# Performance work log

Hardware: AMD Instinct MI355X
Metric: run time of the kernel (lower is better)

The kernel has to match this reference:

```python
import jax, jax.numpy as jnp
import numpy as np

N, E, B = 10000, 160000, 16
IN, H, A, L, OUT = 16, 64, 8, 2, 1
MSG_IN = 2 * (H + 1) + 1   # 131 = concat(x_i, x_j, additional_message_features)
UPD_IN = H + 1 + H         # 129 = concat(x_aug, aggregated message)


def _tp(h, a, W, b):
    # scalar-irreps fully-connected O3 tensor product == bilinear map + bias
    return jnp.einsum('ni,nj,ijk->nk', h, a, W) + b


def setup_inputs() -> dict:
    key = jax.random.key(0)
    ks = jax.random.split(key, 24)
    f32 = jnp.float32
    def rn(k, shape, scale=1.0):
        return jax.random.normal(k, shape, f32) * scale
    def w(k, shape):
        fan = shape[-3] * shape[-2]
        return rn(k, shape, 1.0 / np.sqrt(fan))
    return {
        'x': rn(ks[0], (N, IN)),
        'edge_index': jax.random.randint(ks[1], (2, E), 0, N),
        'edge_attr': rn(ks[2], (E, A)),
        'node_attr': rn(ks[3], (N, A)),
        'additional_message_features': rn(ks[4], (E, 1)),
        'additional_node_features': rn(ks[5], (N, 1)),
        'batch': jnp.sort(jax.random.randint(ks[6], (N,), 0, B)),
        'W_emb': w(ks[7], (IN + 1, A, H)), 'b_emb': jnp.zeros((H,), f32),
        'Wm1': w(ks[8], (L, MSG_IN, A, H)), 'bm1': jnp.zeros((L, H), f32),
        'Wm2': w(ks[9], (L, H, A, H)), 'bm2': jnp.zeros((L, H), f32),
        'Wu1': w(ks[10], (L, UPD_IN, A, H)), 'bu1': jnp.zeros((L, H), f32),
        'Wu2': w(ks[11], (L, H, A, H)), 'bu2': jnp.zeros((L, H), f32),
        'Wp1': w(ks[12], (H, A, H)), 'bp1': jnp.zeros((H,), f32),
        'Wp2': w(ks[13], (H, A, H)), 'bp2': jnp.zeros((H,), f32),
        'Wq1': rn(ks[14], (H, H), 1.0 / np.sqrt(H)), 'bq1': jnp.zeros((H,), f32),
        'Wq2': rn(ks[15], (H, OUT), 1.0 / np.sqrt(H)), 'bq2': jnp.zeros((OUT,), f32),
    }


def _forward(x, edge_attr, node_attr, amf, anf,
             W_emb, b_emb, Wm1, bm1, Wm2, bm2, Wu1, bu1, Wu2, bu2,
             Wp1, bp1, Wp2, bp2, Wq1, bq1, Wq2, bq2, edge_index, batch):
    silu = jax.nn.silu
    src, dst = edge_index[0], edge_index[1]  # source_to_target: aggregate at dst
    n = x.shape[0]
    # embedding: concat additional node features, bilinear TP with node_attr
    h = _tp(jnp.concatenate([x, anf], -1), node_attr, W_emb, b_emb)          # [N,H]
    for l in range(Wm1.shape[0]):  # loop over structurally distinct layers
        h_aug = jnp.concatenate([h, anf], -1)                                # [N,H+1]
        m_in = jnp.concatenate([h_aug[dst], h_aug[src], amf], -1)            # [E,MSG_IN]
        m = silu(_tp(m_in, edge_attr, Wm1[l], bm1[l]))                       # TP + swish gate
        m = silu(_tp(m, edge_attr, Wm2[l], bm2[l]))                          # sg2=True -> gated too
        agg = jax.ops.segment_sum(m, dst, num_segments=n)                    # scatter-add [N,H]
        u = silu(_tp(jnp.concatenate([h_aug, agg], -1), node_attr, Wu1[l], bu1[l]))
        u = _tp(u, node_attr, Wu2[l], bu2[l])                                # no gate on 2nd TP
        h = h + u                                                            # residual, adnid stripped
    # pre-pool MLP (SwishGate TP then plain TP)
    p = silu(_tp(h, node_attr, Wp1, bp1))
    p = _tp(p, node_attr, Wp2, bp2)                                          # [N,POOL=H]
    # global mean pool over graphs
    counts = jax.ops.segment_sum(jnp.ones((n,), p.dtype), batch, num_segments=B)
    g = jax.ops.segment_sum(p, batch, num_segments=B) / jnp.maximum(counts, 1.0)[:, None]
    # post-pool: TP with trivial 1x0e attr == plain linear
    g = silu(g @ Wq1 + bq1)
    return g @ Wq2 + bq2                                                     # [B,OUT]


def reference(x, edge_index, edge_attr, node_attr, additional_message_features,
              additional_node_features, batch, W_emb, b_emb, Wm1, bm1, Wm2, bm2,
              Wu1, bu1, Wu2, bu2, Wp1, bp1, Wp2, bp2, Wq1, bq1, Wq2, bq2):
    return _forward(x, edge_attr, node_attr, additional_message_features,
                    additional_node_features, W_emb, b_emb, Wm1, bm1, Wm2, bm2,
                    Wu1, bu1, Wu2, bu2, Wp1, bp1, Wp2, bp2, Wq1, bq1, Wq2, bq2,
                    edge_index, batch)
```

## Files before the change

### kernel.cpp

```cpp
#include <hip/hip_runtime.h>
#include <hip/hip_bf16.h>
#include <math.h>

constexpr int N = 10000;
constexpr int E = 160000;
constexpr int B = 16;
constexpr int POOL_CHUNKS = 80;
constexpr int MS = 72;
constexpr int HS = 96;

typedef short bf16x8 __attribute__((ext_vector_type(8)));
typedef short bf16x4 __attribute__((ext_vector_type(4)));
typedef float f32x4 __attribute__((ext_vector_type(4)));

__device__ __forceinline__ float silu_f(float x) {
    return x / (1.0f + __expf(-x));
}
__device__ __forceinline__ float bf2f(short s) {
    union { unsigned u; float f; } c; c.u = (unsigned)(unsigned short)s << 16; return c.f;
}

__global__ __launch_bounds__(256) void k_w2(
        const float* __restrict__ Wsrc,
        __hip_bfloat16* __restrict__ Whi, __hip_bfloat16* __restrict__ Wlo) {
    int idx = blockIdx.x * 256 + threadIdx.x;
    int l = idx >> 15;
    int rem = idx & 32767;
    int kk = rem >> 11;
    int nt = (rem >> 9) & 3;
    int c  = (rem >> 5) & 15;
    int q  = (rem >> 3) & 3;
    int j  = rem & 7;
    int i = q * 16 + kk;
    int k = nt * 16 + c;
    float wv = Wsrc[(size_t)l * 32768 + i * 512 + j * 64 + k];
    __hip_bfloat16 hi = __float2bfloat16(wv);
    Whi[idx] = hi;
    Wlo[idx] = __float2bfloat16(wv - __bfloat162float(hi));
}

__global__ __launch_bounds__(256) void k_w2h(
        const float* __restrict__ Wsrc, __hip_bfloat16* __restrict__ Whi) {
    int idx = blockIdx.x * 256 + threadIdx.x;
    int l = idx >> 15;
    int rem = idx & 32767;
    int kk = rem >> 11;
    int nt = (rem >> 9) & 3;
    int c  = (rem >> 5) & 15;
    int q  = (rem >> 3) & 3;
    int j  = rem & 7;
    int i = q * 16 + kk;
    int k = nt * 16 + c;
    Whi[idx] = __float2bfloat16(Wsrc[(size_t)l * 32768 + i * 512 + j * 64 + k]);
}

__global__ __launch_bounds__(256) void k_wu1(
        const float* __restrict__ Wu1,
        __hip_bfloat16* __restrict__ Whi, __hip_bfloat16* __restrict__ Wlo) {
    int idx = blockIdx.x * 256 + threadIdx.x;
    int l = idx / 67584;
    int rem = idx % 67584;
    int kk = rem / 2048;
    int r2 = rem % 2048;
    int nt = (r2 >> 9) & 3;
    int c  = (r2 >> 5) & 15;
    int q  = (r2 >> 3) & 3;
    int j  = r2 & 7;
    int i = q * 33 + kk;
    float wv = (i < 129) ? Wu1[(size_t)l * 129 * 512 + i * 512 + j * 64 + nt * 16 + c] : 0.f;
    __hip_bfloat16 hi = __float2bfloat16(wv);
    Whi[idx] = hi;
    Wlo[idx] = __float2bfloat16(wv - __bfloat162float(hi));
}

__global__ __launch_bounds__(256) void k_wm1z(
        const float* __restrict__ Wm1, __hip_bfloat16* __restrict__ Whi) {
    int idx = blockIdx.x * 256 + threadIdx.x;
    int l = idx / 71680;
    int rem = idx % 71680;
    int kkn = rem >> 9;
    int off = rem & 511;
    int kk = kkn >> 2;
    int nt = kkn & 3;
    int c16 = off >> 5;
    int q = (off >> 3) & 3;
    int j = off & 7;
    int k = nt * 16 + c16;
    int wi = -1;
    if (kk < 17) { int i = q * 17 + kk; if (i <= 64) wi = i; }
    else if (kk < 34) { int s = q * 17 + (kk - 17); if (s <= 64) wi = 65 + s; }
    else { if (q == 0) wi = 130; }
    float wv = (wi >= 0) ? Wm1[((size_t)l * 131 + wi) * 512 + j * 64 + k] : 0.f;
    Whi[idx] = __float2bfloat16(wv);
}

__global__ __launch_bounds__(256) void k_zero_i(int* __restrict__ p, int n) {
    int i = blockIdx.x * 256 + threadIdx.x;
    if (i < n) p[i] = 0;
}

__global__ __launch_bounds__(256) void k_hist(
        const int* __restrict__ eidx, int* __restrict__ hist) {
    int e = blockIdx.x * 256 + threadIdx.x;
    if (e < E) atomicAdd(&hist[eidx[E + e]], 1);
}

__global__ __launch_bounds__(1024) void k_scan(
        const int* __restrict__ hist, int* __restrict__ cursor) {
    __shared__ int wsum[16];
    int t = threadIdx.x;
    int base = t * 10;
    int loc[10];
    int s = 0;
#pragma unroll
    for (int i = 0; i < 10; ++i) {
        int v = (base + i < N) ? hist[base + i] : 0;
        loc[i] = s;
        s += v;
    }
    int lane = t & 63, w = t >> 6;
    int incl = s;
    for (int off = 1; off < 64; off <<= 1) {
        int u = __shfl_up(incl, off, 64);
        if (lane >= off) incl += u;
    }
    if (lane == 63) wsum[w] = incl;
    __syncthreads();
    if (t == 0) {
        int a = 0;
        for (int i2 = 0; i2 < 16; ++i2) { int v = wsum[i2]; wsum[i2] = a; a += v; }
    }
    __syncthreads();
    int excl = incl - s + wsum[w];
#pragma unroll
    for (int i = 0; i < 10; ++i) {
        int p = base + i;
        if (p < N) cursor[p] = excl + loc[i];
    }
}

__global__ __launch_bounds__(256) void k_scatter(
        const int* __restrict__ eidx, int* __restrict__ cursor, int* __restrict__ perm) {
    int e = blockIdx.x * 256 + threadIdx.x;
    if (e < E) {
        int d = eidx[E + e];
        int p = atomicAdd(&cursor[d], 1);
        perm[p] = e;
    }
}

__device__ __forceinline__ void zgemm_stage(
        const __hip_bfloat16* xsrc, int xstride, int kkmax, int Lq,
        int w, int c16, int q, int lofs, const float* naA,
        const __hip_bfloat16* __restrict__ Whi, const __hip_bfloat16* __restrict__ Wlo,
        float (*part_s)[16][64]) {
    f32x4 zero4 = {0.f, 0.f, 0.f, 0.f};
    f32x4 acc[4];
#pragma unroll
    for (int nt = 0; nt < 4; ++nt) acc[nt] = zero4;
    for (int kk = w; kk < kkmax; kk += 4) {
        bf16x8 bh[4], bl[4];
#pragma unroll
        for (int nt = 0; nt < 4; ++nt) {
            int off = (kk * 4 + nt) * 512 + lofs;
            bh[nt] = *(const bf16x8*)(Whi + off);
            bl[nt] = *(const bf16x8*)(Wlo + off);
        }
        float mv = __bfloat162float(xsrc[c16 * xstride + q * Lq + kk]);
        union { bf16x8 v; __hip_bfloat16 hx[8]; } au;
#pragma unroll
        for (int j = 0; j < 8; ++j) au.hx[j] = __float2bfloat16(mv * naA[j]);
#pragma unroll
        for (int nt = 0; nt < 4; ++nt) {
            acc[nt] = __builtin_amdgcn_mfma_f32_16x16x32_bf16(au.v, bh[nt], acc[nt], 0, 0, 0);
            acc[nt] = __builtin_amdgcn_mfma_f32_16x16x32_bf16(au.v, bl[nt], acc[nt], 0, 0, 0);
        }
    }
#pragma unroll
    for (int nt = 0; nt < 4; ++nt)
#pragma unroll
        for (int r = 0; r < 4; ++r) part_s[w][q * 4 + r][nt * 16 + c16] = acc[nt][r];
}

__global__ __launch_bounds__(256) void k_embed_hb(
        const float* __restrict__ x, const float* __restrict__ anf,
        const float* __restrict__ na, const float* __restrict__ W_emb,
        const float* __restrict__ b_emb,
        float* __restrict__ h, __hip_bfloat16* __restrict__ hb, float* __restrict__ agg) {
    __shared__ float xs[16][18];
    __shared__ float na_s[16][8];
    int tid = threadIdx.x, w = tid >> 6, l = tid & 63;
    int n0 = blockIdx.x * 16;
    {
        int r = tid >> 4, c = tid & 15;
        xs[r][c] = x[(size_t)(n0 + r) * 16 + c];
    }
    if (tid < 16) xs[tid][16] = anf[n0 + tid];
    if (tid < 128) na_s[tid >> 3][tid & 7] = na[(size_t)n0 * 8 + tid];
    float4 z4 = {0.f, 0.f, 0.f, 0.f};
    ((float4*)(agg + (size_t)blockIdx.x * 1024))[tid] = z4;
    for (int t = tid; t < 192; t += 256)
        ((float4*)(hb + (size_t)n0 * HS))[t] = z4;
    __syncthreads();
    float acc[4];
#pragma unroll
    for (int t = 0; t < 4; ++t) acc[t] = b_emb[l];
    for (int i = 0; i < 17; ++i) {
#pragma unroll
        for (int j = 0; j < 8; ++j) {
            float wv = W_emb[(i * 8 + j) * 64 + l];
#pragma unroll
            for (int t = 0; t < 4; ++t) {
                int nn = w * 4 + t;
                acc[t] = fmaf(xs[nn][i] * na_s[nn][j], wv, acc[t]);
            }
        }
    }
    int slot = (l / 17) * 24 + l % 17;
#pragma unroll
    for (int t = 0; t < 4; ++t) {
        int n = n0 + w * 4 + t;
        h[(size_t)n * 64 + l] = acc[t];
        hb[(size_t)n * HS + slot] = __float2bfloat16(acc[t]);
    }
    if (tid < 16) hb[(size_t)(n0 + tid) * HS + 85] = __float2bfloat16(xs[tid][16]);
}

__global__ __launch_bounds__(256, 4) void k_edge(
        const int* __restrict__ eidx, const float* __restrict__ ea,
        const float* __restrict__ amf, const int* __restrict__ perm,
        const __hip_bfloat16* __restrict__ hb,
        const __hip_bfloat16* __restrict__ W1hi, const float* __restrict__ bm1_l,
        const __hip_bfloat16* __restrict__ W2hi,
        const float* __restrict__ bm2_l, float* __restrict__ agg) {
    __shared__ __align__(16) char smem_u[128 * 66 * 4];
    __shared__ float amf_s[128];
    __shared__ int src_s[128], dst_s[128];
    __shared__ float bm1_s[64], bm2_s[64];
    float* ea_s = (float*)smem_u;
    __hip_bfloat16* m_s = (__hip_bfloat16*)(smem_u + 4608);
    float* m2 = (float*)smem_u;

    int tid = threadIdx.x;
    int l = tid & 63, w = tid >> 6;
    int e0 = blockIdx.x * 128;
    for (int idx = tid; idx < 128; idx += 256) {
        int pe = perm[e0 + idx];
        src_s[idx] = eidx[pe];
        dst_s[idx] = eidx[E + pe];
        amf_s[idx] = amf[pe];
    }
    for (int idx = tid; idx < 1024; idx += 256) {
        int pe = perm[e0 + (idx >> 3)];
        ea_s[(idx >> 3) * 9 + (idx & 7)] = ea[(size_t)pe * 8 + (idx & 7)];
    }
    if (tid < 64) { bm1_s[tid] = bm1_l[tid]; bm2_s[tid] = bm2_l[tid]; }
    __syncthreads();

    int c16 = l & 15, q = l >> 4;
    int e0w = w * 32;
    float eaA[2][8];
    float amfA[2];
#pragma unroll
    for (int mt = 0; mt < 2; ++mt) {
#pragma unroll
        for (int j = 0; j < 8; ++j) eaA[mt][j] = ea_s[(e0w + mt * 16 + c16) * 9 + j];
        amfA[mt] = amf_s[e0w + mt * 16 + c16];
    }
    int lofs = (c16 * 4 + q) * 8;
    f32x4 zero4 = {0.f, 0.f, 0.f, 0.f};

    bf16x4 xD[2][5], xS[2][5];
#pragma unroll
    for (int mt = 0; mt < 2; ++mt) {
        const __hip_bfloat16* bd = hb + (size_t)dst_s[e0w + mt * 16 + c16] * HS + q * 24;
        const __hip_bfloat16* bs = hb + (size_t)src_s[e0w + mt * 16 + c16] * HS + q * 24;
#pragma unroll
        for (int t = 0; t < 5; ++t) {
            xD[mt][t] = *(const bf16x4*)(bd + t * 4);
            xS[mt][t] = *(const bf16x4*)(bs + t * 4);
        }
    }

    f32x4 acc1[2][4];
#pragma unroll
    for (int mt = 0; mt < 2; ++mt)
#pragma unroll
        for (int nt = 0; nt < 4; ++nt) acc1[mt][nt] = zero4;
#pragma unroll
    for (int kk = 0; kk < 17; ++kk) {
        bf16x8 bh[4];
#pragma unroll
        for (int nt = 0; nt < 4; ++nt)
            bh[nt] = *(const bf16x8*)(W1hi + (kk * 4 + nt) * 512 + lofs);
#pragma unroll
        for (int mt = 0; mt < 2; ++mt) {
            float xv = bf2f(xD[mt][kk >> 2][kk & 3]);
            union { bf16x8 v; __hip_bfloat16 hx[8]; } au;
#pragma unroll
            for (int j = 0; j < 8; ++j) au.hx[j] = __float2bfloat16(xv * eaA[mt][j]);
#pragma unroll
            for (int nt = 0; nt < 4; ++nt)
                acc1[mt][nt] = __builtin_amdgcn_mfma_f32_16x16x32_bf16(au.v, bh[nt], acc1[mt][nt], 0, 0, 0);
        }
    }
#pragma unroll
    for (int kk = 0; kk < 17; ++kk) {
        bf16x8 bh[4];
#pragma unroll
        for (int nt = 0; nt < 4; ++nt)
            bh[nt] = *(const bf16x8*)(W1hi + ((17 + kk) * 4 + nt) * 512 + lofs);
#pragma unroll
        for (int mt = 0; mt < 2; ++mt) {
            float xv = bf2f(xS[mt][kk >> 2][kk & 3]);
            union { bf16x8 v; __hip_bfloat16 hx[8]; } au;
#pragma unroll
            for (int j = 0; j < 8; ++j) au.hx[j] = __float2bfloat16(xv * eaA[mt][j]);
#pragma unroll
            for (int nt = 0; nt < 4; ++nt)
                acc1[mt][nt] = __builtin_amdgcn_mfma_f32_16x16x32_bf16(au.v, bh[nt], acc1[mt][nt], 0, 0, 0);
        }
    }
    {
        bf16x8 bh[4];
#pragma unroll
        for (int nt = 0; nt < 4; ++nt)
            bh[nt] = *(const bf16x8*)(W1hi + (34 * 4 + nt) * 512 + lofs);
#pragma unroll
        for (int mt = 0; mt < 2; ++mt) {
            float xv = (q == 0) ? amfA[mt] : 0.f;
            union { bf16x8 v; __hip_bfloat16 hx[8]; } au;
#pragma unroll
            for (int j = 0; j < 8; ++j) au.hx[j] = __float2bfloat16(xv * eaA[mt][j]);
#pragma unroll
            for (int nt = 0; nt < 4; ++nt)
                acc1[mt][nt] = __builtin_amdgcn_mfma_f32_16x16x32_bf16(au.v, bh[nt], acc1[mt][nt], 0, 0, 0);
        }
    }
#pragma unroll
    for (int mt = 0; mt < 2; ++mt)
#pragma unroll
        for (int nt = 0; nt < 4; ++nt) {
            int kd = nt * 16 + c16;
            float bias = bm1_s[kd];
#pragma unroll
            for (int r = 0; r < 4; ++r) {
                int e = e0w + mt * 16 + q * 4 + r;
                m_s[e * MS + kd] = __float2bfloat16(silu_f(bias + acc1[mt][nt][r]));
            }
        }

    bf16x4 mR[2][4];
#pragma unroll
    for (int mt = 0; mt < 2; ++mt)
#pragma unroll
        for (int t = 0; t < 4; ++t)
            mR[mt][t] = *(const bf16x4*)&m_s[(e0w + mt * 16 + c16) * MS + q * 16 + t * 4];

    __syncthreads();

    f32x4 acc[2][4];
#pragma unroll
    for (int mt = 0; mt < 2; ++mt)
#pragma unroll
        for (int nt = 0; nt < 4; ++nt) acc[mt][nt] = zero4;
#pragma unroll
    for (int kk = 0; kk < 16; ++kk) {
        bf16x8 bh[4];
#pragma unroll
        for (int nt = 0; nt < 4; ++nt)
            bh[nt] = *(const bf16x8*)(W2hi + (kk * 4 + nt) * 512 + lofs);
#pragma unroll
        for (int mt = 0; mt < 2; ++mt) {
            float mv = bf2f(mR[mt][kk >> 2][kk & 3]);
            union { bf16x8 v; __hip_bfloat16 h[8]; } au;
#pragma unroll
            for (int j = 0; j < 8; ++j) au.h[j] = __float2bfloat16(mv * eaA[mt][j]);
#pragma unroll
            for (int nt = 0; nt < 4; ++nt)
                acc[mt][nt] = __builtin_amdgcn_mfma_f32_16x16x32_bf16(au.v, bh[nt], acc[mt][nt], 0, 0, 0);
        }
    }
#pragma unroll
    for (int mt = 0; mt < 2; ++mt)
#pragma unroll
        for (int nt = 0; nt < 4; ++nt) {
            int kd = nt * 16 + c16;
            float bias = bm2_s[kd];
#pragma unroll
            for (int r = 0; r < 4; ++r) {
                int e = e0w + mt * 16 + q * 4 + r;
                m2[e * 66 + kd] = silu_f(bias + acc[mt][nt][r]);
            }
        }

    {
        int r0 = w * 32;
        float run = 0.f;
        int cur_d = dst_s[r0];
        for (int e = r0; e < r0 + 32; ++e) {
            int d = dst_s[e];
            if (d != cur_d) {
                atomicAdd(&agg[(size_t)cur_d * 64 + l], run);
                run = 0.f;
                cur_d = d;
            }
            run += m2[e * 66 + l];
        }
        atomicAdd(&agg[(size_t)cur_d * 64 + l], run);
    }
}

__global__ __launch_bounds__(256) void k_upd_hb(
        const float* __restrict__ h_in, const float* __restrict__ anf,
        const float* __restrict__ na, const float* __restrict__ agg_in,
        const __hip_bfloat16* __restrict__ W1hi, const __hip_bfloat16* __restrict__ W1lo,
        const float* __restrict__ bu1_l,
        const __hip_bfloat16* __restrict__ W2hi_, const __hip_bfloat16* __restrict__ W2lo_,
        const float* __restrict__ bu2_l,
        float* __restrict__ h, __hip_bfloat16* __restrict__ hb, float* __restrict__ agg) {
    __shared__ __align__(16) __hip_bfloat16 xa_s[16 * 136];
    __shared__ __align__(16) __hip_bfloat16 u1_s[16 * 72];
    __shared__ float part_s[4][16][64];
    int tid = threadIdx.x;
    int w = tid >> 6, l = tid & 63;
    int n0 = blockIdx.x * 16;
    for (int idx = tid; idx < 16 * 132; idx += 256) {
        int r = idx / 132, c = idx % 132;
        int n = n0 + r;
        float v;
        if (c < 64) v = h_in[(size_t)n * 64 + c];
        else if (c == 64) v = anf[n];
        else if (c < 129) v = agg_in[(size_t)n * 64 + (c - 65)];
        else v = 0.f;
        xa_s[r * 136 + c] = __float2bfloat16(v);
    }
    int c16 = l & 15, q = l >> 4;
    float naA[8];
#pragma unroll
    for (int j = 0; j < 8; ++j) naA[j] = na[(size_t)(n0 + c16) * 8 + j];
    __syncthreads();
    float4 z4 = {0.f, 0.f, 0.f, 0.f};
    ((float4*)(agg + (size_t)blockIdx.x * 1024))[tid] = z4;
    for (int t = tid; t < 192; t += 256)
        ((float4*)(hb + (size_t)n0 * HS))[t] = z4;
    int lofs = (c16 * 4 + q) * 8;
    zgemm_stage(xa_s, 136, 33, 33, w, c16, q, lofs, naA, W1hi, W1lo, part_s);
    __syncthreads();
    for (int t = tid; t < 1024; t += 256) {
        int row = t >> 6, col = t & 63;
        float v = part_s[0][row][col] + part_s[1][row][col] + part_s[2][row][col] +
                  part_s[3][row][col] + bu1_l[col];
        u1_s[row * 72 + col] = __float2bfloat16(silu_f(v));
    }
    __syncthreads();
    zgemm_stage(u1_s, 72, 16, 16, w, c16, q, lofs, naA, W2hi_, W2lo_, part_s);
    __syncthreads();
    for (int t = tid; t < 1024; t += 256) {
        int row = t >> 6, col = t & 63;
        float v = part_s[0][row][col] + part_s[1][row][col] + part_s[2][row][col] +
                  part_s[3][row][col] + bu2_l[col];
        int n = n0 + row;
        float hn = h[(size_t)n * 64 + col] + v;
        h[(size_t)n * 64 + col] = hn;
        hb[(size_t)n * HS + (col / 17) * 24 + col % 17] = __float2bfloat16(hn);
    }
    if (tid < 16) hb[(size_t)(n0 + tid) * HS + 85] = __float2bfloat16(anf[n0 + tid]);
}

__global__ __launch_bounds__(256) void k_upd_prepool(
        const float* __restrict__ h_in, const float* __restrict__ anf,
        const float* __restrict__ na, const float* __restrict__ agg_in,
        const __hip_bfloat16* __restrict__ W1hi, const __hip_bfloat16* __restrict__ W1lo,
        const float* __restrict__ bu1_l,
        const __hip_bfloat16* __restrict__ W2hi_, const __hip_bfloat16* __restrict__ W2lo_,
        const float* __restrict__ bu2_l,
        const __hip_bfloat16* __restrict__ Wp1hi, const __hip_bfloat16* __restrict__ Wp1lo,
        const float* __restrict__ bp1,
        const __hip_bfloat16* __restrict__ Wp2hi, const __hip_bfloat16* __restrict__ Wp2lo,
        const float* __restrict__ bp2,
        float* __restrict__ p2) {
    __shared__ __align__(16) __hip_bfloat16 xa_s[16 * 136];
    __shared__ __align__(16) __hip_bfloat16 u1_s[16 * 72];
    __shared__ __align__(16) __hip_bfloat16 x2_s[16 * 72];
    __shared__ float part_s[4][16][64];
    int tid = threadIdx.x;
    int w = tid >> 6, l = tid & 63;
    int n0 = blockIdx.x * 16;
    for (int idx = tid; idx < 16 * 132; idx += 256) {
        int r = idx / 132, c = idx % 132;
        int n = n0 + r;
        float v;
        if (c < 64) v = h_in[(size_t)n * 64 + c];
        else if (c == 64) v = anf[n];
        else if (c < 129) v = agg_in[(size_t)n * 64 + (c - 65)];
        else v = 0.f;
        xa_s[r * 136 + c] = __float2bfloat16(v);
    }
    int c16 = l & 15, q = l >> 4;
    float naA[8];
#pragma unroll
    for (int j = 0; j < 8; ++j) naA[j] = na[(size_t)(n0 + c16) * 8 + j];
    __syncthreads();
    int lofs = (c16 * 4 + q) * 8;
    zgemm_stage(xa_s, 136, 33, 33, w, c16, q, lofs, naA, W1hi, W1lo, part_s);
    __syncthreads();
    for (int t = tid; t < 1024; t += 256) {
        int row = t >> 6, col = t & 63;
        float v = part_s[0][row][col] + part_s[1][row][col] + part_s[2][row][col] +
                  part_s[3][row][col] + bu1_l[col];
        u1_s[row * 72 + col] = __float2bfloat16(silu_f(v));
    }
    __syncthreads();
    zgemm_stage(u1_s, 72, 16, 16, w, c16, q, lofs, naA, W2hi_, W2lo_, part_s);
    __syncthreads();
    for (int t = tid; t < 1024; t += 256) {
        int row = t >> 6, col = t & 63;
        float v = part_s[0][row][col] + part_s[1][row][col] + part_s[2][row][col] +
                  part_s[3][row][col] + bu2_l[col];
        float hn = h_in[(size_t)(n0 + row) * 64 + col] + v;
        x2_s[row * 72 + col] = __float2bfloat16(hn);
    }
    __syncthreads();
    zgemm_stage(x2_s, 72, 16, 16, w, c16, q, lofs, naA, Wp1hi, Wp1lo, part_s);
    __syncthreads();
    for (int t = tid; t < 1024; t += 256) {
        int row = t >> 6, col = t & 63;
        float v = part_s[0][row][col] + part_s[1][row][col] + part_s[2][row][col] +
                  part_s[3][row][col] + bp1[col];
        u1_s[row * 72 + col] = __float2bfloat16(silu_f(v));
    }
    __syncthreads();
    zgemm_stage(u1_s, 72, 16, 16, w, c16, q, lofs, naA, Wp2hi, Wp2lo, part_s);
    __syncthreads();
    for (int t = tid; t < 1024; t += 256) {
        int row = t >> 6, col = t & 63;
        float v = part_s[0][row][col] + part_s[1][row][col] + part_s[2][row][col] +
                  part_s[3][row][col] + bp2[col];
        p2[(size_t)(n0 + row) * 64 + col] = v;
    }
}

__global__ __launch_bounds__(256) void k_pool(
        const float* __restrict__ p2, const int* __restrict__ batch,
        float* __restrict__ partial_p, float* __restrict__ partial_cnt) {
    __shared__ float acc_s[16 * 64];
    __shared__ float cnt_s[16];
    int tid = threadIdx.x;
    for (int idx = tid; idx < 1024; idx += 256) acc_s[idx] = 0.f;
    if (tid < 16) cnt_s[tid] = 0.f;
    __syncthreads();
    int w = tid >> 6, k = tid & 63;
    int base = blockIdx.x * 125;
    for (int i = 0; i < 32; ++i) {
        int nl = i * 4 + w;
        if (nl < 125) {
            int n = base + nl;
            int b = batch[n];
            atomicAdd(&acc_s[b * 64 + k], p2[(size_t)n * 64 + k]);
            if (k == 0) atomicAdd(&cnt_s[b], 1.0f);
        }
    }
    __syncthreads();
    for (int idx = tid; idx < 1024; idx += 256)
        partial_p[(size_t)blockIdx.x * 1024 + idx] = acc_s[idx];
    if (tid < 16) partial_cnt[blockIdx.x * 16 + tid] = cnt_s[tid];
}

__global__ __launch_bounds__(1024) void k_final(
        const float* __restrict__ partial_p, const float* __restrict__ partial_cnt,
        const float* __restrict__ Wq1, const float* __restrict__ bq1,
        const float* __restrict__ Wq2, const float* __restrict__ bq2,
        float* __restrict__ out) {
    __shared__ float g[16][64];
    int b = threadIdx.x >> 6, k = threadIdx.x & 63;
    float s = 0.f, cc = 0.f;
    for (int c = 0; c < POOL_CHUNKS; ++c) s += partial_p[(size_t)c * 1024 + b * 64 + k];
    for (int c = 0; c < POOL_CHUNKS; ++c) cc += partial_cnt[c * 16 + b];
    g[b][k] = s / fmaxf(cc, 1.0f);
    __syncthreads();
    float acc = bq1[k];
#pragma unroll
    for (int i = 0; i < 64; ++i) acc = fmaf(g[b][i], Wq1[i * 64 + k], acc);
    float v = silu_f(acc) * Wq2[k];
#pragma unroll
    for (int off = 32; off > 0; off >>= 1) v += __shfl_down(v, off, 64);
    if (k == 0) out[b] = v + bq2[0];
}

extern "C" void kernel_launch(void* const* d_in, const int* in_sizes, int n_in,
                              void* d_out, int out_size, void* d_ws, size_t ws_size,
                              hipStream_t stream) {
    const float* x    = (const float*)d_in[0];
    const int*   eidx = (const int*)  d_in[1];
    const float* ea   = (const float*)d_in[2];
    const float* na   = (const float*)d_in[3];
    const float* amf  = (const float*)d_in[4];
    const float* anf  = (const float*)d_in[5];
    const int*   batch= (const int*)  d_in[6];
    const float* W_emb= (const float*)d_in[7];
    const float* b_emb= (const float*)d_in[8];
    const float* Wm1  = (const float*)d_in[9];
    const float* bm1  = (const float*)d_in[10];
    const float* Wm2  = (const float*)d_in[11];
    const float* bm2  = (const float*)d_in[12];
    const float* Wu1  = (const float*)d_in[13];
    const float* bu1  = (const float*)d_in[14];
    const float* Wu2  = (const float*)d_in[15];
    const float* bu2  = (const float*)d_in[16];
    const float* Wp1  = (const float*)d_in[17];
    const float* bp1  = (const float*)d_in[18];
    const float* Wp2  = (const float*)d_in[19];
    const float* bp2  = (const float*)d_in[20];
    const float* Wq1  = (const float*)d_in[21];
    const float* bq1  = (const float*)d_in[22];
    const float* Wq2  = (const float*)d_in[23];
    const float* bq2  = (const float*)d_in[24];

    float* ws = (float*)d_ws;
    float* h      = ws;
    float* agg    = h + (size_t)N * 64;
    float* p2     = agg + (size_t)N * 64;
    float* part_p = p2 + (size_t)N * 64;
    float* part_c = part_p + POOL_CHUNKS * 1024;
    float* fend   = part_c + POOL_CHUNKS * 16;
    __hip_bfloat16* hb     = (__hip_bfloat16*)fend;
    __hip_bfloat16* W2hi   = hb + (size_t)N * HS;
    __hip_bfloat16* Wm1zhi = W2hi + 65536;
    __hip_bfloat16* Wu1hi  = Wm1zhi + 143360;
    __hip_bfloat16* Wu1lo  = Wu1hi + 135168;
    __hip_bfloat16* Wu2hi  = Wu1lo + 135168;
    __hip_bfloat16* Wu2lo  = Wu2hi + 65536;
    __hip_bfloat16* Wp1hi  = Wu2lo + 65536;
    __hip_bfloat16* Wp1lo  = Wp1hi + 32768;
    __hip_bfloat16* Wp2hi  = Wp1lo + 32768;
    __hip_bfloat16* Wp2lo  = Wp2hi + 32768;
    int* hist   = (int*)(Wp2lo + 32768);
    int* cursor = hist + N;
    int* perm   = cursor + N;

    k_zero_i<<<(N + 255) / 256, 256, 0, stream>>>(hist, N);
    k_hist<<<(E + 255) / 256, 256, 0, stream>>>(eidx, hist);
    k_scan<<<1, 1024, 0, stream>>>(hist, cursor);
    k_scatter<<<(E + 255) / 256, 256, 0, stream>>>(eidx, cursor, perm);

    k_w2h<<<256, 256, 0, stream>>>(Wm2, W2hi);
    k_wm1z<<<560, 256, 0, stream>>>(Wm1, Wm1zhi);
    k_wu1<<<528, 256, 0, stream>>>(Wu1, Wu1hi, Wu1lo);
    k_w2<<<256, 256, 0, stream>>>(Wu2, Wu2hi, Wu2lo);
    k_w2<<<128, 256, 0, stream>>>(Wp1, Wp1hi, Wp1lo);
    k_w2<<<128, 256, 0, stream>>>(Wp2, Wp2hi, Wp2lo);

    k_embed_hb<<<625, 256, 0, stream>>>(x, anf, na, W_emb, b_emb, h, hb, agg);
    k_edge<<<E / 128, 256, 0, stream>>>(eidx, ea, amf, perm, hb,
                                        Wm1zhi, bm1, W2hi, bm2, agg);
    k_upd_hb<<<625, 256, 0, stream>>>(h, anf, na, agg,
                                      Wu1hi, Wu1lo, bu1,
                                      Wu2hi, Wu2lo, bu2,
                                      h, hb, agg);
    k_edge<<<E / 128, 256, 0, stream>>>(eidx, ea, amf, perm, hb,
                                        Wm1zhi + 71680, bm1 + 64,
                                        W2hi + 32768, bm2 + 64, agg);
    k_upd_prepool<<<625, 256, 0, stream>>>(h, anf, na, agg,
                                           Wu1hi + 67584, Wu1lo + 67584, bu1 + 64,
                                           Wu2hi + 32768, Wu2lo + 32768, bu2 + 64,
                                           Wp1hi, Wp1lo, bp1, Wp2hi, Wp2lo, bp2, p2);
    k_pool<<<POOL_CHUNKS, 256, 0, stream>>>(p2, batch, part_p, part_c);
    k_final<<<1, 1024, 0, stream>>>(part_p, part_c, Wq1, bq1, Wq2, bq2, (float*)d_out);
}
```

Measured before the change: 392.5 us.

## Merge prep kernels into one launch and pre-sort edge data by destination

The weight-conversion kernels, the histogram zeroing and the node embedding are folded into a single block-partitioned kernel, cutting the launch count. The scatter step now writes src, dst, amf and edge attributes in dst-sorted order, so the two edge kernels read them contiguously instead of gathering through a permutation and staging them in shared memory. Bias values move into registers, and edge-kernel shared memory shrinks. The cost is extra global buffers and a heavier scatter kernel that does uncoalesced writes.

```diff
diff --git a/kernel.cpp b/kernel.cpp
--- a/kernel.cpp
+++ b/kernel.cpp
@@ -20,10 +20,9 @@
     union { unsigned u; float f; } c; c.u = (unsigned)(unsigned short)s << 16; return c.f;
 }
 
-__global__ __launch_bounds__(256) void k_w2(
-        const float* __restrict__ Wsrc,
+__device__ __forceinline__ void w2_body(
+        int idx, const float* __restrict__ Wsrc,
         __hip_bfloat16* __restrict__ Whi, __hip_bfloat16* __restrict__ Wlo) {
-    int idx = blockIdx.x * 256 + threadIdx.x;
     int l = idx >> 15;
     int rem = idx & 32767;
     int kk = rem >> 11;
@@ -39,9 +38,8 @@
     Wlo[idx] = __float2bfloat16(wv - __bfloat162float(hi));
 }
 
-__global__ __launch_bounds__(256) void k_w2h(
-        const float* __restrict__ Wsrc, __hip_bfloat16* __restrict__ Whi) {
-    int idx = blockIdx.x * 256 + threadIdx.x;
+__device__ __forceinline__ void w2h_body(
+        int idx, const float* __restrict__ Wsrc, __hip_bfloat16* __restrict__ Whi) {
     int l = idx >> 15;
     int rem = idx & 32767;
     int kk = rem >> 11;
@@ -54,10 +52,9 @@
     Whi[idx] = __float2bfloat16(Wsrc[(size_t)l * 32768 + i * 512 + j * 64 + k]);
 }
 
-__global__ __launch_bounds__(256) void k_wu1(
-        const float* __restrict__ Wu1,
+__device__ __forceinline__ void wu1_body(
+        int idx, const float* __restrict__ Wu1,
         __hip_bfloat16* __restrict__ Whi, __hip_bfloat16* __restrict__ Wlo) {
-    int idx = blockIdx.x * 256 + threadIdx.x;
     int l = idx / 67584;
     int rem = idx % 67584;
     int kk = rem / 2048;
@@ -73,9 +70,8 @@
     Wlo[idx] = __float2bfloat16(wv - __bfloat162float(hi));
 }
 
-__global__ __launch_bounds__(256) void k_wm1z(
-        const float* __restrict__ Wm1, __hip_bfloat16* __restrict__ Whi) {
-    int idx = blockIdx.x * 256 + threadIdx.x;
+__device__ __forceinline__ void wm1z_body(
+        int idx, const float* __restrict__ Wm1, __hip_bfloat16* __restrict__ Whi) {
     int l = idx / 71680;
     int rem = idx % 71680;
     int kkn = rem >> 9;
@@ -94,9 +90,85 @@
     Whi[idx] = __float2bfloat16(wv);
 }
 
-__global__ __launch_bounds__(256) void k_zero_i(int* __restrict__ p, int n) {
-    int i = blockIdx.x * 256 + threadIdx.x;
-    if (i < n) p[i] = 0;
+constexpr int PB_W2H  = 0;
+constexpr int PB_WM1Z = PB_W2H  + 256;
+constexpr int PB_WU1  = PB_WM1Z + 560;
+constexpr int PB_WU2  = PB_WU1  + 528;
+constexpr int PB_WP1  = PB_WU2  + 256;
+constexpr int PB_WP2  = PB_WP1  + 128;
+constexpr int PB_ZERO = PB_WP2  + 128;
+constexpr int PB_EMB  = PB_ZERO + 40;
+constexpr int PB_TOTAL= PB_EMB  + 625;
+
+__global__ __launch_bounds__(256) void k_pre(
+        const float* __restrict__ Wm2, __hip_bfloat16* __restrict__ W2hi,
+        const float* __restrict__ Wm1, __hip_bfloat16* __restrict__ Wm1zhi,
+        const float* __restrict__ Wu1w, __hip_bfloat16* __restrict__ Wu1hi, __hip_bfloat16* __restrict__ Wu1lo,
+        const float* __restrict__ Wu2w, __hip_bfloat16* __restrict__ Wu2hi, __hip_bfloat16* __restrict__ Wu2lo,
+        const float* __restrict__ Wp1w, __hip_bfloat16* __restrict__ Wp1hi, __hip_bfloat16* __restrict__ Wp1lo,
+        const float* __restrict__ Wp2w, __hip_bfloat16* __restrict__ Wp2hi, __hip_bfloat16* __restrict__ Wp2lo,
+        int* __restrict__ hist,
+        const float* __restrict__ x, const float* __restrict__ anf,
+        const float* __restrict__ na, const float* __restrict__ W_emb,
+        const float* __restrict__ b_emb,
+        float* __restrict__ h, __hip_bfloat16* __restrict__ hb, float* __restrict__ agg) {
+    __shared__ float xs[16][18];
+    __shared__ float na_s[16][8];
+    int tid = threadIdx.x;
+    int bx = blockIdx.x;
+    if (bx < PB_WM1Z) {
+        w2h_body((bx - PB_W2H) * 256 + tid, Wm2, W2hi);
+    } else if (bx < PB_WU1) {
+        wm1z_body((bx - PB_WM1Z) * 256 + tid, Wm1, Wm1zhi);
+    } else if (bx < PB_WU2) {
+        wu1_body((bx - PB_WU1) * 256 + tid, Wu1w, Wu1hi, Wu1lo);
+    } else if (bx < PB_WP1) {
+        w2_body((bx - PB_WU2) * 256 + tid, Wu2w, Wu2hi, Wu2lo);
+    } else if (bx < PB_WP2) {
+        w2_body((bx - PB_WP1) * 256 + tid, Wp1w, Wp1hi, Wp1lo);
+    } else if (bx < PB_ZERO) {
+        w2_body((bx - PB_WP2) * 256 + tid, Wp2w, Wp2hi, Wp2lo);
+    } else if (bx < PB_EMB) {
+        int i = (bx - PB_ZERO) * 256 + tid;
+        if (i < N) hist[i] = 0;
+    } else {
+        int eb = bx - PB_EMB;
+        int w = tid >> 6, l = tid & 63;
+        int n0 = eb * 16;
+        {
+            int r = tid >> 4, c = tid & 15;
+            xs[r][c] = x[(size_t)(n0 + r) * 16 + c];
+        }
+        if (tid < 16) xs[tid][16] = anf[n0 + tid];
+        if (tid < 128) na_s[tid >> 3][tid & 7] = na[(size_t)n0 * 8 + tid];
+        float4 z4 = {0.f, 0.f, 0.f, 0.f};
+        ((float4*)(agg + (size_t)eb * 1024))[tid] = z4;
+        for (int t = tid; t < 192; t += 256)
+            ((float4*)(hb + (size_t)n0 * HS))[t] = z4;
+        __syncthreads();
+        float acc[4];
+#pragma unroll
+        for (int t = 0; t < 4; ++t) acc[t] = b_emb[l];
+        for (int i = 0; i < 17; ++i) {
+#pragma unroll
+            for (int j = 0; j < 8; ++j) {
+                float wv = W_emb[(i * 8 + j) * 64 + l];
+#pragma unroll
+                for (int t = 0; t < 4; ++t) {
+                    int nn = w * 4 + t;
+                    acc[t] = fmaf(xs[nn][i] * na_s[nn][j], wv, acc[t]);
+                }
+            }
+        }
+        int slot = (l / 17) * 24 + l % 17;
+#pragma unroll
+        for (int t = 0; t < 4; ++t) {
+            int n = n0 + w * 4 + t;
+            h[(size_t)n * 64 + l] = acc[t];
+            hb[(size_t)n * HS + slot] = __float2bfloat16(acc[t]);
+        }
+        if (tid < 16) hb[(size_t)(n0 + tid) * HS + 85] = __float2bfloat16(xs[tid][16]);
+    }
 }
 
 __global__ __launch_bounds__(256) void k_hist(
@@ -139,13 +211,22 @@
     }
 }
 
-__global__ __launch_bounds__(256) void k_scatter(
-        const int* __restrict__ eidx, int* __restrict__ cursor, int* __restrict__ perm) {
+__global__ __launch_bounds__(256) void k_scatter_sort(
+        const int* __restrict__ eidx, const float* __restrict__ ea,
+        const float* __restrict__ amf, int* __restrict__ cursor,
+        int* __restrict__ srcS, int* __restrict__ dstS,
+        float* __restrict__ amfS, float* __restrict__ eaS) {
     int e = blockIdx.x * 256 + threadIdx.x;
     if (e < E) {
         int d = eidx[E + e];
         int p = atomicAdd(&cursor[d], 1);
-        perm[p] = e;
+        srcS[p] = eidx[e];
+        dstS[p] = d;
+        amfS[p] = amf[e];
+        float4 a0 = ((const float4*)ea)[(size_t)e * 2];
+        float4 a1 = ((const float4*)ea)[(size_t)e * 2 + 1];
+        ((float4*)eaS)[(size_t)p * 2] = a0;
+        ((float4*)eaS)[(size_t)p * 2 + 1] = a1;
     }
 }
 
@@ -182,90 +263,43 @@
         for (int r = 0; r < 4; ++r) part_s[w][q * 4 + r][nt * 16 + c16] = acc[nt][r];
 }
 
-__global__ __launch_bounds__(256) void k_embed_hb(
-        const float* __restrict__ x, const float* __restrict__ anf,
-        const float* __restrict__ na, const float* __restrict__ W_emb,
-        const float* __restrict__ b_emb,
-        float* __restrict__ h, __hip_bfloat16* __restrict__ hb, float* __restrict__ agg) {
-    __shared__ float xs[16][18];
-    __shared__ float na_s[16][8];
-    int tid = threadIdx.x, w = tid >> 6, l = tid & 63;
-    int n0 = blockIdx.x * 16;
-    {
-        int r = tid >> 4, c = tid & 15;
-        xs[r][c] = x[(size_t)(n0 + r) * 16 + c];
-    }
-    if (tid < 16) xs[tid][16] = anf[n0 + tid];
-    if (tid < 128) na_s[tid >> 3][tid & 7] = na[(size_t)n0 * 8 + tid];
-    float4 z4 = {0.f, 0.f, 0.f, 0.f};
-    ((float4*)(agg + (size_t)blockIdx.x * 1024))[tid] = z4;
-    for (int t = tid; t < 192; t += 256)
-        ((float4*)(hb + (size_t)n0 * HS))[t] = z4;
-    __syncthreads();
-    float acc[4];
-#pragma unroll
-    for (int t = 0; t < 4; ++t) acc[t] = b_emb[l];
-    for (int i = 0; i < 17; ++i) {
-#pragma unroll
-        for (int j = 0; j < 8; ++j) {
-            float wv = W_emb[(i * 8 + j) * 64 + l];
-#pragma unroll
-            for (int t = 0; t < 4; ++t) {
-                int nn = w * 4 + t;
-                acc[t] = fmaf(xs[nn][i] * na_s[nn][j], wv, acc[t]);
-            }
-        }
-    }
-    int slot = (l / 17) * 24 + l % 17;
-#pragma unroll
-    for (int t = 0; t < 4; ++t) {
-        int n = n0 + w * 4 + t;
-        h[(size_t)n * 64 + l] = acc[t];
-        hb[(size_t)n * HS + slot] = __float2bfloat16(acc[t]);
-    }
-    if (tid < 16) hb[(size_t)(n0 + tid) * HS + 85] = __float2bfloat16(xs[tid][16]);
-}
-
 __global__ __launch_bounds__(256, 4) void k_edge(
-        const int* __restrict__ eidx, const float* __restrict__ ea,
-        const float* __restrict__ amf, const int* __restrict__ perm,
+        const int* __restrict__ srcS, const int* __restrict__ dstS,
+        const float* __restrict__ amfS, const float* __restrict__ eaS,
         const __hip_bfloat16* __restrict__ hb,
         const __hip_bfloat16* __restrict__ W1hi, const float* __restrict__ bm1_l,
         const __hip_bfloat16* __restrict__ W2hi,
         const float* __restrict__ bm2_l, float* __restrict__ agg) {
     __shared__ __align__(16) char smem_u[128 * 66 * 4];
-    __shared__ float amf_s[128];
-    __shared__ int src_s[128], dst_s[128];
-    __shared__ float bm1_s[64], bm2_s[64];
-    float* ea_s = (float*)smem_u;
-    __hip_bfloat16* m_s = (__hip_bfloat16*)(smem_u + 4608);
+    __shared__ int dst_s[128];
+    __hip_bfloat16* m_s = (__hip_bfloat16*)smem_u;
     float* m2 = (float*)smem_u;
 
     int tid = threadIdx.x;
     int l = tid & 63, w = tid >> 6;
     int e0 = blockIdx.x * 128;
-    for (int idx = tid; idx < 128; idx += 256) {
-        int pe = perm[e0 + idx];
-        src_s[idx] = eidx[pe];
-        dst_s[idx] = eidx[E + pe];
-        amf_s[idx] = amf[pe];
-    }
-    for (int idx = tid; idx < 1024; idx += 256) {
-        int pe = perm[e0 + (idx >> 3)];
-        ea_s[(idx >> 3) * 9 + (idx & 7)] = ea[(size_t)pe * 8 + (idx & 7)];
-    }
-    if (tid < 64) { bm1_s[tid] = bm1_l[tid]; bm2_s[tid] = bm2_l[tid]; }
-    __syncthreads();
+    if (tid < 128) dst_s[tid] = dstS[e0 + tid];
 
     int c16 = l & 15, q = l >> 4;
     int e0w = w * 32;
-    float eaA[2][8];
-    float amfA[2];
+    float eaA[2][8], amfA[2];
+    int dL[2], sL[2];
 #pragma unroll
     for (int mt = 0; mt < 2; ++mt) {
-#pragma unroll
-        for (int j = 0; j < 8; ++j) eaA[mt][j] = ea_s[(e0w + mt * 16 + c16) * 9 + j];
-        amfA[mt] = amf_s[e0w + mt * 16 + c16];
+        int e = e0 + e0w + mt * 16 + c16;
+        float4 a0 = ((const float4*)eaS)[(size_t)e * 2];
+        float4 a1 = ((const float4*)eaS)[(size_t)e * 2 + 1];
+        eaA[mt][0] = a0.x; eaA[mt][1] = a0.y; eaA[mt][2] = a0.z; eaA[mt][3] = a0.w;
+        eaA[mt][4] = a1.x; eaA[mt][5] = a1.y; eaA[mt][6] = a1.z; eaA[mt][7] = a1.w;
+        amfA[mt] = amfS[e];
+        dL[mt] = dstS[e];
+        sL[mt] = srcS[e];
+    }
+    float bR1[4], bR2[4];
+#pragma unroll
+    for (int nt = 0; nt < 4; ++nt) {
+        bR1[nt] = bm1_l[nt * 16 + c16];
+        bR2[nt] = bm2_l[nt * 16 + c16];
     }
     int lofs = (c16 * 4 + q) * 8;
     f32x4 zero4 = {0.f, 0.f, 0.f, 0.f};
@@ -273,8 +307,8 @@
     bf16x4 xD[2][5], xS[2][5];
 #pragma unroll
     for (int mt = 0; mt < 2; ++mt) {
-        const __hip_bfloat16* bd = hb + (size_t)dst_s[e0w + mt * 16 + c16] * HS + q * 24;
-        const __hip_bfloat16* bs = hb + (size_t)src_s[e0w + mt * 16 + c16] * HS + q * 24;
+        const __hip_bfloat16* bd = hb + (size_t)dL[mt] * HS + q * 24;
+        const __hip_bfloat16* bs = hb + (size_t)sL[mt] * HS + q * 24;
 #pragma unroll
         for (int t = 0; t < 5; ++t) {
             xD[mt][t] = *(const bf16x4*)(bd + t * 4);
@@ -342,7 +376,7 @@
 #pragma unroll
         for (int nt = 0; nt < 4; ++nt) {
             int kd = nt * 16 + c16;
-            float bias = bm1_s[kd];
+            float bias = bR1[nt];
 #pragma unroll
             for (int r = 0; r < 4; ++r) {
                 int e = e0w + mt * 16 + q * 4 + r;
@@ -386,7 +420,7 @@
 #pragma unroll
         for (int nt = 0; nt < 4; ++nt) {
             int kd = nt * 16 + c16;
-            float bias = bm2_s[kd];
+            float bias = bR2[nt];
 #pragma unroll
             for (int r = 0; r < 4; ++r) {
                 int e = e0w + mt * 16 + q * 4 + r;
@@ -637,28 +671,28 @@
     __hip_bfloat16* Wp2lo  = Wp2hi + 32768;
     int* hist   = (int*)(Wp2lo + 32768);
     int* cursor = hist + N;
-    int* perm   = cursor + N;
-
-    k_zero_i<<<(N + 255) / 256, 256, 0, stream>>>(hist, N);
+    int* srcS   = cursor + N;
+    int* dstS   = srcS + E;
+    float* amfS = (float*)(dstS + E);
+    float* eaS  = amfS + E;
+
+    k_pre<<<PB_TOTAL, 256, 0, stream>>>(
+        Wm2, W2hi, Wm1, Wm1zhi, Wu1, Wu1hi, Wu1lo, Wu2, Wu2hi, Wu2lo,
+        Wp1, Wp1hi, Wp1lo, Wp2, Wp2hi, Wp2lo, hist,
+        x, anf, na, W_emb, b_emb, h, hb, agg);
+
     k_hist<<<(E + 255) / 256, 256, 0, stream>>>(eidx, hist);
     k_scan<<<1, 1024, 0, stream>>>(hist, cursor);
-    k_scatter<<<(E + 255) / 256, 256, 0, stream>>>(eidx, cursor, perm);
-
-    k_w2h<<<256, 256, 0, stream>>>(Wm2, W2hi);
-    k_wm1z<<<560, 256, 0, stream>>>(Wm1, Wm1zhi);
-    k_wu1<<<528, 256, 0, stream>>>(Wu1, Wu1hi, Wu1lo);
-    k_w2<<<256, 256, 0, stream>>>(Wu2, Wu2hi, Wu2lo);
-    k_w2<<<128, 256, 0, stream>>>(Wp1, Wp1hi, Wp1lo);
-    k_w2<<<128, 256, 0, stream>>>(Wp2, Wp2hi, Wp2lo);
-
-    k_embed_hb<<<625, 256, 0, stream>>>(x, anf, na, W_emb, b_emb, h, hb, agg);
-    k_edge<<<E / 128, 256, 0, stream>>>(eidx, ea, amf, perm, hb,
+    k_scatter_sort<<<(E + 255) / 256, 256, 0, stream>>>(eidx, ea, amf, cursor,
+                                                        srcS, dstS, amfS, eaS);
+
+    k_edge<<<E / 128, 256, 0, stream>>>(srcS, dstS, amfS, eaS, hb,
                                         Wm1zhi, bm1, W2hi, bm2, agg);
     k_upd_hb<<<625, 256, 0, stream>>>(h, anf, na, agg,
                                       Wu1hi, Wu1lo, bu1,
                                       Wu2hi, Wu2lo, bu2,
                                       h, hb, agg);
-    k_edge<<<E / 128, 256, 0, stream>>>(eidx, ea, amf, perm, hb,
+    k_edge<<<E / 128, 256, 0, stream>>>(srcS, dstS, amfS, eaS, hb,
                                         Wm1zhi + 71680, bm1 + 64,
                                         W2hi + 32768, bm2 + 64, agg);
     k_upd_prepool<<<625, 256, 0, stream>>>(h, anf, na, agg,
```

New measurement: 385.8 us. Within noise of the previous version (-1.7%).
